# Performance work log

Measured on AMD Instinct MI355X. Metric: run time of the kernel, lower is better.

The kernel has to match this reference:

```python
import jax, jax.numpy as jnp
import numpy as np
from jax import lax

# ---- module config (init_kwargs) ----
B, CIN, COUT, H, W, K = 16, 32, 32, 256, 256, 3
FEATURE_BITS = 8
INPUT_ZP = 3
OUTPUT_ZP = -5
INPUT_SCALE = 0.02
OUTPUT_SCALE = 0.05
STRIDE = (1, 1)
PAD_H, PAD_W = 1, 1
DILATION = (1, 1)
GROUPS = 1
QMIN, QMAX = -(2 ** (FEATURE_BITS - 1)), 2 ** (FEATURE_BITS - 1) - 1  # -128, 127


def float_to_fixed_point(scale, bitwidth):
    # Represent scale (in (0,1)) as int_scale * 2^-frac_bits with int_scale <= 2^(b-1)-1.
    # Pick the largest frac_bits s.t. round(scale * 2^frac_bits) fits -> max precision.
    qmax = jnp.float32(2 ** (bitwidth - 1) - 1)
    frac_bits = jnp.floor(jnp.log2(qmax / scale)).astype(jnp.int32)
    int_scale = jnp.round(scale * jnp.exp2(frac_bits.astype(jnp.float32))).astype(jnp.int32)
    return int_scale, frac_bits


def setup_inputs() -> dict:
    key = jax.random.key(0)
    k0, k1, k2, k3 = jax.random.split(key, 4)
    x = jax.random.randint(k0, (B, CIN, H, W), -128, 128, dtype=jnp.int32).astype(jnp.int8)
    qweight = jax.random.randint(k1, (COUT, CIN, K, K), -128, 128, dtype=jnp.int32).astype(jnp.int8)
    qbias = jax.random.randint(k2, (COUT,), -1000, 1000, dtype=jnp.int32)
    weight_scale = jax.random.uniform(k3, (COUT,), jnp.float32, 1e-3, 1e-2)
    return {"x": x, "qweight": qweight, "qbias": qbias, "weight_scale": weight_scale}


def reference(x, qweight, qbias, weight_scale):
    # F.pad(qinput, (pw,pw,ph,ph), 'constant', input_zero_point) -> pad W and H dims
    xp = jnp.pad(x, ((0, 0), (0, 0), (PAD_H, PAD_H), (PAD_W, PAD_W)),
                 mode="constant", constant_values=INPUT_ZP)
    # int32 conv (no bias), VALID since input was pre-padded
    out = lax.conv_general_dilated(
        xp.astype(jnp.int32), qweight.astype(jnp.int32),
        window_strides=STRIDE, padding="VALID", rhs_dilation=DILATION,
        dimension_numbers=("NCHW", "OIHW", "NCHW"), feature_group_count=GROUPS)
    # shifted bias: qbias - sum(qweight) * input_zero_point  (per out channel)
    shifted_qbias = qbias - qweight.astype(jnp.int32).sum((1, 2, 3)) * INPUT_ZP
    out = out + shifted_qbias[None, :, None, None]
    # fixed-point requant: (out * int_scale) >> frac_bits, per channel
    folded_scale = (INPUT_SCALE * weight_scale / OUTPUT_SCALE).astype(jnp.float32)
    int_scale, frac_bits = float_to_fixed_point(folded_scale, FEATURE_BITS)
    out = jnp.right_shift(out * int_scale[None, :, None, None],
                          frac_bits[None, :, None, None])  # arithmetic shift on int32
    out = out + OUTPUT_ZP
    out = jnp.clip(out, QMIN, QMAX).astype(jnp.int8)
    return out
```

## Files before the change

kernel.cpp:

```cpp
#include <hip/hip_runtime.h>

#define B_   16
#define CIN  32
#define COUT 32
#define H_   256
#define W_   256
#define IN_ZP  3
#define OUT_ZP (-5)
#define HW (H_ * W_)
#define TH 8
#define TW 64
#define SW 72
#define SH 10

using i32x4  = __attribute__((ext_vector_type(4))) int;
using i32x16 = __attribute__((ext_vector_type(16))) int;

__global__ void qconv_prep(const int* __restrict__ qw, const int* __restrict__ qb,
                           const float* __restrict__ wscale, int* __restrict__ ws) {
    const int co  = blockIdx.x;
    const int tid = threadIdx.x;
    __shared__ int red[4];
    const int* wco = qw + co * (CIN * 9);

    int s = 0;
    for (int i = tid; i < CIN * 9; i += 256) s += wco[i];
    for (int off = 32; off; off >>= 1) s += __shfl_down(s, off, 64);
    if ((tid & 63) == 0) red[tid >> 6] = s;

    if (tid < 72) {
        int gidx = blockIdx.x * 72 + tid;
        int g    = gidx & 3;
        int lane = (gidx >> 2) & 63;
        int t    = gidx >> 8;
        int wco2 = lane & 31;
        int ci0  = 16 * (lane >> 5) + 4 * g;
        const int* base = qw + wco2 * (CIN * 9);
        int b0 = base[(ci0 + 0) * 9 + t] & 0xff;
        int b1 = base[(ci0 + 1) * 9 + t] & 0xff;
        int b2 = base[(ci0 + 2) * 9 + t] & 0xff;
        int b3 = base[(ci0 + 3) * 9 + t] & 0xff;
        ws[gidx] = b0 | (b1 << 8) | (b2 << 16) | (b3 << 24);
    }
    __syncthreads();
    if (tid == 0) {
        int wsum = red[0] + red[1] + red[2] + red[3];
        ws[2304 + co] = qb[co] - wsum * IN_ZP;
        float fs = (0.02f * wscale[co]) / 0.05f;
        float fb = floorf(log2f(127.0f / fs));
        ws[2336 + co] = (int)rintf(fs * exp2f(fb));
        ws[2368 + co] = (int)fb;
    }
}

__device__ __forceinline__ void stage_item(int idx, int ht, int wt,
                                           const int* __restrict__ xb,
                                           int (*smem)[SH][SW]) {
    int cig = idx / 180;
    int rem = idx - cig * 180;
    int r   = rem / 18;
    int c4  = rem - r * 18;
    int gh  = ht - 1 + r;
    int gw0 = wt - 4 + c4 * 4;
    int ghc = min(H_ - 1, max(0, gh));
    int gwc = min(W_ - 4, max(0, gw0));
    const int* p = xb + (cig * 4) * HW + ghc * W_ + gwc;
    i32x4 v0 = *(const i32x4*)(p);
    i32x4 v1 = *(const i32x4*)(p + HW);
    i32x4 v2 = *(const i32x4*)(p + 2 * HW);
    i32x4 v3 = *(const i32x4*)(p + 3 * HW);
    bool vh = (unsigned)gh < (unsigned)H_;
    i32x4 pk;
#pragma unroll
    for (int j = 0; j < 4; ++j) {
        int t = (v0[j] & 0xff) | ((v1[j] & 0xff) << 8) |
                ((v2[j] & 0xff) << 16) | (v3[j] << 24);
        bool ok = vh && ((unsigned)(gw0 + j) < (unsigned)W_);
        pk[j] = ok ? t : 0x03030303;
    }
    *(i32x4*)&smem[cig][r][c4 * 4] = pk;
}

__global__ __launch_bounds__(256) void qconv_fused(const int* __restrict__ x,
                                                   const int* __restrict__ ws,
                                                   int* __restrict__ out) {
    __shared__ int smem[8][SH][SW];
    __shared__ int scr[4][33 * 32];
    const int wt = blockIdx.x * TW;
    const int ht = blockIdx.y * TH;
    const int b  = blockIdx.z;
    const int tid = threadIdx.x;
    const int* xb = x + b * (CIN * HW);

    stage_item(tid,        ht, wt, xb, smem);
    stage_item(tid + 256,  ht, wt, xb, smem);
    stage_item(tid + 512,  ht, wt, xb, smem);
    stage_item(tid + 768,  ht, wt, xb, smem);
    stage_item(tid + 1024, ht, wt, xb, smem);
    if (tid < 160) stage_item(tid + 1280, ht, wt, xb, smem);
    __syncthreads();

    const int lane = tid & 63, wv = tid >> 6;
    const int co = lane & 31, hh = lane >> 5;

    i32x4 bfrag[9];
    const i32x4* bws = (const i32x4*)ws;
#pragma unroll
    for (int t = 0; t < 9; ++t) bfrag[t] = bws[t * 64 + lane];

    const int sb  = ws[2304 + co];
    const int isc = ws[2336 + co];
    const int fb  = ws[2368 + co];

    int* myscr = &scr[wv][0];
    const int w_r   = lane & 31;
    const int cbase = lane >> 5;

#pragma unroll
    for (int i = 0; i < 4; ++i) {
        int mt = wv * 4 + i;
        int r0 = mt >> 1, chunk = mt & 1;
        i32x16 acc;
#pragma unroll
        for (int r = 0; r < 16; ++r) acc[r] = sb;
#pragma unroll
        for (int t = 0; t < 9; ++t) {
            int dh = t / 3, dw = t % 3;
            int rr = r0 + dh;
            int c  = chunk * 32 + (lane & 31) + dw + 3;
            i32x4 a;
#pragma unroll
            for (int g = 0; g < 4; ++g) a[g] = smem[4 * hh + g][rr][c];
            acc = __builtin_amdgcn_mfma_i32_32x32x32_i8(a, bfrag[t], acc, 0, 0, 0);
        }
#pragma unroll
        for (int rg = 0; rg < 4; ++rg)
#pragma unroll
            for (int j = 0; j < 4; ++j) {
                int t2 = (int)((unsigned)acc[rg * 4 + j] * (unsigned)isc) >> fb;
                t2 += OUT_ZP;
                t2 = min(127, max(-128, t2));
                myscr[co * 33 + (4 * hh + 8 * rg + j)] = t2;
            }
        int* op = out + (b * COUT) * HW + (ht + r0) * W_ + wt + chunk * 32 + w_r;
#pragma unroll
        for (int it = 0; it < 16; ++it) {
            int co_r = 2 * it + cbase;
            op[co_r * HW] = myscr[co_r * 33 + w_r];
        }
    }
}

extern "C" void kernel_launch(void* const* d_in, const int* in_sizes, int n_in,
                              void* d_out, int out_size, void* d_ws, size_t ws_size,
                              hipStream_t stream) {
    const int*   x   = (const int*)d_in[0];
    const int*   qw  = (const int*)d_in[1];
    const int*   qb  = (const int*)d_in[2];
    const float* wsc = (const float*)d_in[3];
    int* ws  = (int*)d_ws;
    int* out = (int*)d_out;

    qconv_prep<<<32, 256, 0, stream>>>(qw, qb, wsc, ws);
    dim3 grid(W_ / TW, H_ / TH, B_);
    qconv_fused<<<grid, 256, 0, stream>>>(x, ws, out);
}
```

Before: 251.8 us.

## Swap MFMA operands to store output directly, drop LDS transpose scratch

Swaps the MFMA A/B operands so the accumulator rows index output channels and the lanes index pixels. Each lane can then write coalesced output straight from registers, with no transpose through shared-memory scratch. Per-channel bias and the packed scale/shift are staged once into a small LDS table, and the launch bounds now ask for 6 blocks per CU to raise occupancy. The block index is also remapped to change the order in which tiles are visited across batches, with possible effects on cache locality.

After: 461.3 us. 83.2% more time.

```diff
diff --git a/kernel.cpp b/kernel.cpp
--- a/kernel.cpp
+++ b/kernel.cpp
@@ -48,8 +48,8 @@
         ws[2304 + co] = qb[co] - wsum * IN_ZP;
         float fs = (0.02f * wscale[co]) / 0.05f;
         float fb = floorf(log2f(127.0f / fs));
-        ws[2336 + co] = (int)rintf(fs * exp2f(fb));
-        ws[2368 + co] = (int)fb;
+        int isc = (int)rintf(fs * exp2f(fb));
+        ws[2336 + co] = isc | (((int)fb) << 16);
     }
 }
 
@@ -81,16 +81,24 @@
     *(i32x4*)&smem[cig][r][c4 * 4] = pk;
 }
 
-__global__ __launch_bounds__(256) void qconv_fused(const int* __restrict__ x,
-                                                   const int* __restrict__ ws,
-                                                   int* __restrict__ out) {
+__global__ __launch_bounds__(256, 6) void qconv_fused(const int* __restrict__ x,
+                                                      const int* __restrict__ ws,
+                                                      int* __restrict__ out) {
     __shared__ int smem[8][SH][SW];
-    __shared__ int scr[4][33 * 32];
-    const int wt = blockIdx.x * TW;
-    const int ht = blockIdx.y * TH;
-    const int b  = blockIdx.z;
+    __shared__ __align__(16) int cons[64];
+
+    const int d  = blockIdx.x + 4 * blockIdx.y + 128 * blockIdx.z;
+    const int w  = ((d & 7) << 8) | (d >> 3);
+    const int tx = w & 3;
+    const int ty = (w >> 2) & 31;
+    const int tb = w >> 7;
+
+    const int wt = tx * TW;
+    const int ht = ty * TH;
     const int tid = threadIdx.x;
-    const int* xb = x + b * (CIN * HW);
+    const int* xb = x + tb * (CIN * HW);
+
+    if (tid < 64) cons[tid] = ws[2304 + tid];
 
     stage_item(tid,        ht, wt, xb, smem);
     stage_item(tid + 256,  ht, wt, xb, smem);
@@ -101,52 +109,46 @@
     __syncthreads();
 
     const int lane = tid & 63, wv = tid >> 6;
-    const int co = lane & 31, hh = lane >> 5;
+    const int hh  = lane >> 5;
+    const int pix = lane & 31;
 
-    i32x4 bfrag[9];
-    const i32x4* bws = (const i32x4*)ws;
+    i32x4 wfrag[9];
+    const i32x4* wsv = (const i32x4*)ws;
 #pragma unroll
-    for (int t = 0; t < 9; ++t) bfrag[t] = bws[t * 64 + lane];
-
-    const int sb  = ws[2304 + co];
-    const int isc = ws[2336 + co];
-    const int fb  = ws[2368 + co];
-
-    int* myscr = &scr[wv][0];
-    const int w_r   = lane & 31;
-    const int cbase = lane >> 5;
+    for (int t = 0; t < 9; ++t) wfrag[t] = wsv[t * 64 + lane];
 
 #pragma unroll
     for (int i = 0; i < 4; ++i) {
-        int mt = wv * 4 + i;
-        int r0 = mt >> 1, chunk = mt & 1;
+        const int mt = wv * 4 + i;
+        const int r0 = mt >> 1, chunk = mt & 1;
         i32x16 acc;
 #pragma unroll
-        for (int r = 0; r < 16; ++r) acc[r] = sb;
+        for (int r = 0; r < 16; ++r) acc[r] = 0;
 #pragma unroll
         for (int t = 0; t < 9; ++t) {
-            int dh = t / 3, dw = t % 3;
-            int rr = r0 + dh;
-            int c  = chunk * 32 + (lane & 31) + dw + 3;
+            const int dh = t / 3, dw = t % 3;
+            const int rr = r0 + dh;
+            const int c  = chunk * 32 + pix + dw + 3;
             i32x4 a;
 #pragma unroll
             for (int g = 0; g < 4; ++g) a[g] = smem[4 * hh + g][rr][c];
-            acc = __builtin_amdgcn_mfma_i32_32x32x32_i8(a, bfrag[t], acc, 0, 0, 0);
+            acc = __builtin_amdgcn_mfma_i32_32x32x32_i8(wfrag[t], a, acc, 0, 0, 0);
         }
+        int* op = out + (tb * COUT) * HW + (ht + r0) * W_ + wt + chunk * 32 + pix;
 #pragma unroll
-        for (int rg = 0; rg < 4; ++rg)
+        for (int rg = 0; rg < 4; ++rg) {
+            const int cb = 4 * hh + 8 * rg;
+            i32x4 sb4 = *(const i32x4*)&cons[cb];
+            i32x4 qf4 = *(const i32x4*)&cons[32 + cb];
 #pragma unroll
             for (int j = 0; j < 4; ++j) {
-                int t2 = (int)((unsigned)acc[rg * 4 + j] * (unsigned)isc) >> fb;
-                t2 += OUT_ZP;
-                t2 = min(127, max(-128, t2));
-                myscr[co * 33 + (4 * hh + 8 * rg + j)] = t2;
+                int q = qf4[j];
+                int v = acc[rg * 4 + j] + sb4[j];
+                v = (int)((unsigned)v * (unsigned)(q & 0xffff)) >> (q >> 16);
+                v += OUT_ZP;
+                v = min(127, max(-128, v));
+                op[(cb + j) * HW] = v;
             }
-        int* op = out + (b * COUT) * HW + (ht + r0) * W_ + wt + chunk * 32 + w_r;
-#pragma unroll
-        for (int it = 0; it < 16; ++it) {
-            int co_r = 2 * it + cbase;
-            op[co_r * HW] = myscr[co_r * 33 + w_r];
         }
     }
 }
```
